# Optimization experiments

Measured on AMD Instinct MI355X. Metric: run time of the kernel, lower is better.

The kernel has to match this reference:

```python
import jax, jax.numpy as jnp
import numpy as np

N_SRC, N_DST, DEG = 100000, 50000, 16
NODE_IN, EDGE_IN, HID = 128, 64, 64
E = N_DST * DEG


def sparsemax(z):
    # z: [..., K]; sparsemax along last axis (Martins & Astudillo)
    z = z - jnp.max(z, axis=-1, keepdims=True)
    zs = -jnp.sort(-z, axis=-1)  # descending sort
    k_range = jnp.arange(1, z.shape[-1] + 1, dtype=z.dtype)
    cs = jnp.cumsum(zs, axis=-1)
    is_gt = (1.0 + k_range * zs > cs).astype(z.dtype)
    k = jnp.max(is_gt * k_range, axis=-1, keepdims=True)
    tau = (jnp.sum(is_gt * zs, axis=-1, keepdims=True) - 1.0) / k
    return jnp.maximum(z - tau, 0.0)


def setup_inputs() -> dict:
    key = jax.random.key(0)
    ks = jax.random.split(key, 8)
    s = 0.02
    return {
        "node_features": jax.random.normal(ks[0], (N_SRC, NODE_IN), jnp.float32),
        "edge_features": jax.random.normal(ks[1], (E, EDGE_IN), jnp.float32),
        "src_idx": jax.random.randint(ks[2], (E,), 0, N_SRC, jnp.int32),
        "We": s * jax.random.normal(ks[3], (EDGE_IN, HID), jnp.float32),
        "be": jnp.zeros((HID,), jnp.float32),
        "Wa": s * jax.random.normal(ks[4], (EDGE_IN, HID), jnp.float32),
        "ba": jnp.zeros((HID,), jnp.float32),
        "wa": s * jax.random.normal(ks[5], (HID,), jnp.float32),
        "Wo": s * jax.random.normal(ks[6], (NODE_IN + HID, HID), jnp.float32),
        "bo": jnp.zeros((HID,), jnp.float32),
        "Wn": s * jax.random.normal(ks[7], (NODE_IN + HID, HID), jnp.float32),
        "bn": jnp.zeros((HID,), jnp.float32),
        "n_dst": N_DST,
        "deg": DEG,
    }


def reference(node_features, edge_features, src_idx, We, be, Wa, ba, wa, Wo, bo, Wn, bn, n_dst, deg):
    # dropout is identity in eval / p=0
    h_dst = node_features[:n_dst]                               # [n_dst, node_in]
    # message_func: per-edge transforms
    e_out = jax.nn.relu(edge_features @ We + be)                # [E, hid]
    a = jax.nn.leaky_relu((edge_features @ Wa + ba) @ wa)       # [E]
    h_src_e = node_features[src_idx]                            # gather [E, node_in]
    m = jax.nn.relu(jnp.concatenate([h_src_e, e_out], axis=-1) @ Wo + bo)  # [E, hid]
    # reduce_func: mailbox is [n_dst, deg, .] (fixed in-degree graph)
    a = a.reshape(n_dst, deg)
    m = m.reshape(n_dst, deg, -1)
    alpha = sparsemax(a)                                        # [n_dst, deg]
    h_neigh = jnp.einsum('nd,ndh->nh', alpha, m)                # [n_dst, hid]
    # node update
    return jax.nn.relu(jnp.concatenate([h_dst, h_neigh], axis=-1) @ Wn + bn)
```

## Files before the change

kernel.cpp:

```cpp
#include <hip/hip_runtime.h>


#define ND 50000

typedef __bf16 bf16x8 __attribute__((ext_vector_type(8)));
typedef float f32x4 __attribute__((ext_vector_type(4)));

__device__ __forceinline__ void sync_wave() {
  asm volatile("s_waitcnt lgkmcnt(0)" ::: "memory");
}

__device__ __forceinline__ unsigned short f2bf(float x) {
  unsigned u = __float_as_uint(x);
  u += 0x7fffu + ((u >> 16) & 1u);
  return (unsigned short)(u >> 16);
}

union FragU { bf16x8 v; unsigned short u[8]; };

__device__ __forceinline__ bf16x8 ld_cvt8(const float* __restrict__ p, float* fr) {
  float4 f0 = *reinterpret_cast<const float4*>(p);
  float4 f1 = *reinterpret_cast<const float4*>(p + 4);
  fr[0]=f0.x; fr[1]=f0.y; fr[2]=f0.z; fr[3]=f0.w;
  fr[4]=f1.x; fr[5]=f1.y; fr[6]=f1.z; fr[7]=f1.w;
  FragU fu;
  #pragma unroll
  for (int j = 0; j < 8; ++j) fu.u[j] = f2bf(fr[j]);
  return fu.v;
}

extern "C" __global__ void gteast_prep(const float* __restrict__ Wa,
                                       const float* __restrict__ ba,
                                       const float* __restrict__ wa,
                                       float* __restrict__ vc) {
  const int k = threadIdx.x;
  if (k < 64) {
    float s = 0.f;
    for (int h = 0; h < 64; ++h) s += Wa[k * 64 + h] * wa[h];
    vc[k] = s;
  }
  if (k == 0) {
    float c = 0.f;
    for (int h = 0; h < 64; ++h) c += ba[h] * wa[h];
    vc[64] = c;
  }
}

#define MFMA(a, b, c) __builtin_amdgcn_mfma_f32_16x16x32_bf16((a), (b), (c), 0, 0, 0)

extern "C" __global__ void __launch_bounds__(256, 2)
gteast_edge(const float* __restrict__ nf, const float* __restrict__ ef,
            const int* __restrict__ src_idx,
            const float* __restrict__ We, const float* __restrict__ be,
            const float* __restrict__ Wo, const float* __restrict__ bo,
            const float* __restrict__ vc,
            float* __restrict__ hn_out) {
  __shared__ unsigned short WeT[64 * 72];
  __shared__ unsigned short WoT[64 * 200];
  __shared__ unsigned short Elds[4][16 * 72];

  const int tid = threadIdx.x;
  for (int i = tid; i < 64 * 64; i += 256) {
    int k = i >> 6, n = i & 63;
    WeT[n * 72 + k] = f2bf(We[i]);
  }
  for (int i = tid; i < 192 * 64; i += 256) {
    int k = i >> 6, n = i & 63;
    WoT[n * 200 + k] = f2bf(Wo[i]);
  }
  __syncthreads();

  const int lane = tid & 63, w = tid >> 6;
  const int q = lane >> 4, t = lane & 15;

  bf16x8 WeF[2][4], WoF[6][4];
  #pragma unroll
  for (int nt = 0; nt < 4; ++nt) {
    #pragma unroll
    for (int kc = 0; kc < 2; ++kc)
      WeF[kc][nt] = *reinterpret_cast<const bf16x8*>(&WeT[(nt * 16 + t) * 72 + kc * 32 + q * 8]);
    #pragma unroll
    for (int kc = 0; kc < 6; ++kc)
      WoF[kc][nt] = *reinterpret_cast<const bf16x8*>(&WoT[(nt * 16 + t) * 200 + kc * 32 + q * 8]);
  }
  float vsl[16];
  #pragma unroll
  for (int kc = 0; kc < 2; ++kc)
    for (int j = 0; j < 8; ++j) vsl[kc * 8 + j] = vc[kc * 32 + q * 8 + j];
  const float cval = vc[64];
  float beL[4], boL[4];
  #pragma unroll
  for (int nt = 0; nt < 4; ++nt) { beL[nt] = be[nt * 16 + t]; boL[nt] = bo[nt * 16 + t]; }

  unsigned short* E = Elds[w];
  const int wid = blockIdx.x * 4 + w;

  for (int it = 0; it < 8; ++it) {
    const int n = wid + it * 6252;
    if (n >= ND) continue;
    const long e0 = (long)n * 16;

    bf16x8 efr[2];
    float fr[8];
    float ap = 0.f;
    #pragma unroll
    for (int kc = 0; kc < 2; ++kc) {
      efr[kc] = ld_cvt8(ef + (e0 + t) * 64 + kc * 32 + q * 8, fr);
      #pragma unroll
      for (int j = 0; j < 8; ++j) ap += fr[j] * vsl[kc * 8 + j];
    }
    ap += __shfl_xor(ap, 16);
    ap += __shfl_xor(ap, 32);
    float a = ap + cval;
    a = a > 0.f ? a : 0.01f * a;

    #pragma unroll
    for (int nt = 0; nt < 4; ++nt) {
      f32x4 c = {0.f, 0.f, 0.f, 0.f};
      c = MFMA(efr[0], WeF[0][nt], c);
      c = MFMA(efr[1], WeF[1][nt], c);
      #pragma unroll
      for (int r = 0; r < 4; ++r) {
        float vv = fmaxf(c[r] + beL[nt], 0.f);
        E[(4 * q + r) * 72 + nt * 16 + t] = f2bf(vv);
      }
    }
    sync_wave();

    const int s = src_idx[e0 + t];
    const float* hp = nf + (long)s * 128;
    bf16x8 af[6];
    #pragma unroll
    for (int kc = 0; kc < 4; ++kc) af[kc] = ld_cvt8(hp + kc * 32 + q * 8, fr);
    af[4] = *reinterpret_cast<const bf16x8*>(&E[t * 72 + q * 8]);
    af[5] = *reinterpret_cast<const bf16x8*>(&E[t * 72 + 32 + q * 8]);

    f32x4 accM[4];
    #pragma unroll
    for (int nt = 0; nt < 4; ++nt) {
      f32x4 c = {0.f, 0.f, 0.f, 0.f};
      #pragma unroll
      for (int kc = 0; kc < 6; ++kc) c = MFMA(af[kc], WoF[kc][nt], c);
      #pragma unroll
      for (int r = 0; r < 4; ++r) c[r] = fmaxf(c[r] + boL[nt], 0.f);
      accM[nt] = c;
    }
    sync_wave();

    float z = a;
    #pragma unroll
    for (int k = 2; k <= 16; k <<= 1) {
      #pragma unroll
      for (int j = k >> 1; j > 0; j >>= 1) {
        float o = __shfl_xor(z, j);
        const bool upper = (t & j) != 0;
        const bool desc = (t & k) == 0;
        z = (upper != desc) ? fmaxf(z, o) : fminf(z, o);
      }
    }
    float cs = z;
    #pragma unroll
    for (int off = 1; off < 16; off <<= 1) {
      float o = __shfl_up(cs, off, 16);
      cs += (t >= off) ? o : 0.f;
    }
    const bool gt = 1.f + (float)(t + 1) * z > cs;
    float kf = gt ? (float)(t + 1) : 0.f;
    float sv = gt ? z : 0.f;
    #pragma unroll
    for (int m = 1; m < 16; m <<= 1) {
      kf = fmaxf(kf, __shfl_xor(kf, m));
      sv += __shfl_xor(sv, m);
    }
    const float tau = (sv - 1.f) / kf;
    const float alpha = fmaxf(a - tau, 0.f);

    float al[4];
    #pragma unroll
    for (int r = 0; r < 4; ++r) al[r] = __shfl(alpha, 4 * q + r);
    float p[4];
    #pragma unroll
    for (int nt = 0; nt < 4; ++nt) {
      p[nt] = al[0] * accM[nt][0] + al[1] * accM[nt][1] +
              al[2] * accM[nt][2] + al[3] * accM[nt][3];
      p[nt] += __shfl_xor(p[nt], 16);
      p[nt] += __shfl_xor(p[nt], 32);
    }
    const float pown = (q == 0) ? p[0] : (q == 1) ? p[1] : (q == 2) ? p[2] : p[3];
    hn_out[(long)n * 64 + lane] = pown;
  }
}

extern "C" __global__ void __launch_bounds__(256, 2)
gteast_out(const float* __restrict__ nf, const float* __restrict__ Wn,
           const float* __restrict__ bn, float* __restrict__ out) {
  __shared__ unsigned short WnT[64 * 200];
  const int tid = threadIdx.x;
  for (int i = tid; i < 192 * 64; i += 256) {
    int k = i >> 6, nn = i & 63;
    WnT[nn * 200 + k] = f2bf(Wn[i]);
  }
  __syncthreads();

  const int lane = tid & 63, w = tid >> 6, q = lane >> 4, t = lane & 15;
  bf16x8 WF[6][4];
  #pragma unroll
  for (int nt = 0; nt < 4; ++nt)
    #pragma unroll
    for (int kc = 0; kc < 6; ++kc)
      WF[kc][nt] = *reinterpret_cast<const bf16x8*>(&WnT[(nt * 16 + t) * 200 + kc * 32 + q * 8]);
  float bnL[4];
  #pragma unroll
  for (int nt = 0; nt < 4; ++nt) bnL[nt] = bn[nt * 16 + t];

  const int wid = blockIdx.x * 4 + w;
  for (int it = 0; it < 2; ++it) {
    const int tile = wid + it * 1564;
    const int r0 = tile * 16;
    if (r0 >= ND) continue;

    float fr[8];
    bf16x8 af[6];
    const float* hp = nf + (long)(r0 + t) * 128;
    #pragma unroll
    for (int kc = 0; kc < 4; ++kc) af[kc] = ld_cvt8(hp + kc * 32 + q * 8, fr);
    const float* gp = out + (long)(r0 + t) * 64;
    #pragma unroll
    for (int kc = 0; kc < 2; ++kc) af[4 + kc] = ld_cvt8(gp + kc * 32 + q * 8, fr);

    #pragma unroll
    for (int nt = 0; nt < 4; ++nt) {
      f32x4 c = {0.f, 0.f, 0.f, 0.f};
      #pragma unroll
      for (int kc = 0; kc < 6; ++kc) c = MFMA(af[kc], WF[kc][nt], c);
      #pragma unroll
      for (int r = 0; r < 4; ++r)
        out[(long)(r0 + 4 * q + r) * 64 + nt * 16 + t] = fmaxf(c[r] + bnL[nt], 0.f);
    }
  }
}

extern "C" void kernel_launch(void* const* d_in, const int* in_sizes, int n_in,
                              void* d_out, int out_size, void* d_ws, size_t ws_size,
                              hipStream_t stream) {
  const float* nf = (const float*)d_in[0];
  const float* ef = (const float*)d_in[1];
  const int* si   = (const int*)d_in[2];
  const float* We = (const float*)d_in[3];
  const float* be = (const float*)d_in[4];
  const float* Wa = (const float*)d_in[5];
  const float* ba = (const float*)d_in[6];
  const float* wa = (const float*)d_in[7];
  const float* Wo = (const float*)d_in[8];
  const float* bo = (const float*)d_in[9];
  const float* Wn = (const float*)d_in[10];
  const float* bn = (const float*)d_in[11];
  float* out = (float*)d_out;
  float* vc = (float*)d_ws;

  gteast_prep<<<1, 64, 0, stream>>>(Wa, ba, wa, vc);
  gteast_edge<<<1563, 256, 0, stream>>>(nf, ef, si, We, be, Wo, bo, vc, out);
  gteast_out<<<391, 256, 0, stream>>>(nf, Wn, bn, out);
}
```

Measured before the change: 418.5 us.

## Software-pipeline edge/neighbor loads, read weights from LDS, raise occupancy

The edge kernel now gives each wave 8 contiguous destination nodes instead of strided ones. It preloads the src indices once and prefetches the next iteration's edge features and gathered neighbor rows into registers while the current iteration computes. Weight fragments are read from LDS per MFMA instead of being held in registers, which frees VGPRs so launch bounds can go from 2 to 3 blocks per SIMD. Both kernels use a cheaper perm-based bf16 pack that rounds to nearest with ties away from zero instead of to even. The output kernel uses one tile per wave with twice as many blocks, and the prep kernel splits its dot products across 256 threads.

Result: faster. 387.5 us (-7.4%).

```diff
diff --git a/kernel.cpp b/kernel.cpp
--- a/kernel.cpp
+++ b/kernel.cpp
@@ -16,39 +16,41 @@
   return (unsigned short)(u >> 16);
 }
 
-union FragU { bf16x8 v; unsigned short u[8]; };
-
-__device__ __forceinline__ bf16x8 ld_cvt8(const float* __restrict__ p, float* fr) {
-  float4 f0 = *reinterpret_cast<const float4*>(p);
-  float4 f1 = *reinterpret_cast<const float4*>(p + 4);
-  fr[0]=f0.x; fr[1]=f0.y; fr[2]=f0.z; fr[3]=f0.w;
-  fr[4]=f1.x; fr[5]=f1.y; fr[6]=f1.z; fr[7]=f1.w;
-  FragU fu;
-  #pragma unroll
-  for (int j = 0; j < 8; ++j) fu.u[j] = f2bf(fr[j]);
-  return fu.v;
-}
+union Frag8 { bf16x8 v; unsigned u32[4]; };
+
+__device__ __forceinline__ bf16x8 pack8(const float* fr) {
+  Frag8 f;
+  #pragma unroll
+  for (int j = 0; j < 4; ++j) {
+    unsigned lo = __float_as_uint(fr[2 * j]) + 0x8000u;
+    unsigned hi = __float_as_uint(fr[2 * j + 1]) + 0x8000u;
+    f.u32[j] = __builtin_amdgcn_perm(hi, lo, 0x07060302);
+  }
+  return f.v;
+}
+
+#define MFMA(a, b, c) __builtin_amdgcn_mfma_f32_16x16x32_bf16((a), (b), (c), 0, 0, 0)
 
 extern "C" __global__ void gteast_prep(const float* __restrict__ Wa,
                                        const float* __restrict__ ba,
                                        const float* __restrict__ wa,
                                        float* __restrict__ vc) {
-  const int k = threadIdx.x;
-  if (k < 64) {
-    float s = 0.f;
-    for (int h = 0; h < 64; ++h) s += Wa[k * 64 + h] * wa[h];
-    vc[k] = s;
-  }
-  if (k == 0) {
-    float c = 0.f;
-    for (int h = 0; h < 64; ++h) c += ba[h] * wa[h];
-    vc[64] = c;
-  }
-}
-
-#define MFMA(a, b, c) __builtin_amdgcn_mfma_f32_16x16x32_bf16((a), (b), (c), 0, 0, 0)
-
-extern "C" __global__ void __launch_bounds__(256, 2)
+  __shared__ float red[260];
+  const int tid = threadIdx.x, k = tid >> 2, p = tid & 3;
+  float s = 0.f;
+  for (int h = 16 * p; h < 16 * p + 16; ++h) s += Wa[k * 64 + h] * wa[h];
+  red[tid] = s;
+  if (tid < 4) {
+    float sc = 0.f;
+    for (int h = 16 * tid; h < 16 * tid + 16; ++h) sc += ba[h] * wa[h];
+    red[256 + tid] = sc;
+  }
+  __syncthreads();
+  if (p == 0) vc[k] = red[4 * k] + red[4 * k + 1] + red[4 * k + 2] + red[4 * k + 3];
+  if (tid == 0) vc[64] = red[256] + red[257] + red[258] + red[259];
+}
+
+extern "C" __global__ void __launch_bounds__(256, 3)
 gteast_edge(const float* __restrict__ nf, const float* __restrict__ ef,
             const int* __restrict__ src_idx,
             const float* __restrict__ We, const float* __restrict__ be,
@@ -58,6 +60,7 @@
   __shared__ unsigned short WeT[64 * 72];
   __shared__ unsigned short WoT[64 * 200];
   __shared__ unsigned short Elds[4][16 * 72];
+  __shared__ float vls[68];
 
   const int tid = threadIdx.x;
   for (int i = tid; i < 64 * 64; i += 256) {
@@ -68,57 +71,80 @@
     int k = i >> 6, n = i & 63;
     WoT[n * 200 + k] = f2bf(Wo[i]);
   }
+  if (tid < 65) vls[tid] = vc[tid];
   __syncthreads();
 
   const int lane = tid & 63, w = tid >> 6;
   const int q = lane >> 4, t = lane & 15;
-
-  bf16x8 WeF[2][4], WoF[6][4];
-  #pragma unroll
-  for (int nt = 0; nt < 4; ++nt) {
-    #pragma unroll
-    for (int kc = 0; kc < 2; ++kc)
-      WeF[kc][nt] = *reinterpret_cast<const bf16x8*>(&WeT[(nt * 16 + t) * 72 + kc * 32 + q * 8]);
-    #pragma unroll
-    for (int kc = 0; kc < 6; ++kc)
-      WoF[kc][nt] = *reinterpret_cast<const bf16x8*>(&WoT[(nt * 16 + t) * 200 + kc * 32 + q * 8]);
-  }
+  const int wid = blockIdx.x * 4 + w;
+  if (wid * 8 >= ND) return;
+
+  unsigned short* E = Elds[w];
+  const float cval = vls[64];
+  float beL[4], boL[4];
+  #pragma unroll
+  for (int nt = 0; nt < 4; ++nt) { beL[nt] = be[nt * 16 + t]; boL[nt] = bo[nt * 16 + t]; }
   float vsl[16];
   #pragma unroll
-  for (int kc = 0; kc < 2; ++kc)
-    for (int j = 0; j < 8; ++j) vsl[kc * 8 + j] = vc[kc * 32 + q * 8 + j];
-  const float cval = vc[64];
-  float beL[4], boL[4];
-  #pragma unroll
-  for (int nt = 0; nt < 4; ++nt) { beL[nt] = be[nt * 16 + t]; boL[nt] = bo[nt * 16 + t]; }
-
-  unsigned short* E = Elds[w];
-  const int wid = blockIdx.x * 4 + w;
+  for (int j = 0; j < 8; ++j) { vsl[j] = vls[q * 8 + j]; vsl[8 + j] = vls[32 + q * 8 + j]; }
+
+  const int si0 = src_idx[wid * 128 + lane];
+  const int si1 = src_idx[wid * 128 + 64 + lane];
+
+  const long ebase = (long)(wid * 128);
+
+  float4 efn[4];
+  {
+    const float* er = ef + (ebase + t) * 64 + q * 8;
+    efn[0] = *reinterpret_cast<const float4*>(er);
+    efn[1] = *reinterpret_cast<const float4*>(er + 4);
+    efn[2] = *reinterpret_cast<const float4*>(er + 32);
+    efn[3] = *reinterpret_cast<const float4*>(er + 36);
+  }
+  float hraw[32];
+  {
+    const int s0 = __shfl(si0, t);
+    const float* hp = nf + (long)s0 * 128 + q * 8;
+    #pragma unroll
+    for (int kc = 0; kc < 4; ++kc) {
+      float4 a0 = *reinterpret_cast<const float4*>(hp + kc * 32);
+      float4 a1 = *reinterpret_cast<const float4*>(hp + kc * 32 + 4);
+      hraw[kc * 8 + 0] = a0.x; hraw[kc * 8 + 1] = a0.y; hraw[kc * 8 + 2] = a0.z; hraw[kc * 8 + 3] = a0.w;
+      hraw[kc * 8 + 4] = a1.x; hraw[kc * 8 + 5] = a1.y; hraw[kc * 8 + 6] = a1.z; hraw[kc * 8 + 7] = a1.w;
+    }
+  }
 
   for (int it = 0; it < 8; ++it) {
-    const int n = wid + it * 6252;
-    if (n >= ND) continue;
-    const long e0 = (long)n * 16;
-
-    bf16x8 efr[2];
-    float fr[8];
+    const int n = wid * 8 + it;
+    const int itn = it < 7 ? it + 1 : 7;
+
+    float fe[16];
+    fe[0] = efn[0].x; fe[1] = efn[0].y; fe[2] = efn[0].z; fe[3] = efn[0].w;
+    fe[4] = efn[1].x; fe[5] = efn[1].y; fe[6] = efn[1].z; fe[7] = efn[1].w;
+    fe[8] = efn[2].x; fe[9] = efn[2].y; fe[10] = efn[2].z; fe[11] = efn[2].w;
+    fe[12] = efn[3].x; fe[13] = efn[3].y; fe[14] = efn[3].z; fe[15] = efn[3].w;
+    {
+      const float* er = ef + (ebase + itn * 16 + t) * 64 + q * 8;
+      efn[0] = *reinterpret_cast<const float4*>(er);
+      efn[1] = *reinterpret_cast<const float4*>(er + 4);
+      efn[2] = *reinterpret_cast<const float4*>(er + 32);
+      efn[3] = *reinterpret_cast<const float4*>(er + 36);
+    }
+
     float ap = 0.f;
     #pragma unroll
-    for (int kc = 0; kc < 2; ++kc) {
-      efr[kc] = ld_cvt8(ef + (e0 + t) * 64 + kc * 32 + q * 8, fr);
-      #pragma unroll
-      for (int j = 0; j < 8; ++j) ap += fr[j] * vsl[kc * 8 + j];
-    }
+    for (int j = 0; j < 16; ++j) ap += fe[j] * vsl[j];
     ap += __shfl_xor(ap, 16);
     ap += __shfl_xor(ap, 32);
     float a = ap + cval;
     a = a > 0.f ? a : 0.01f * a;
 
+    const bf16x8 e0 = pack8(fe), e1 = pack8(fe + 8);
     #pragma unroll
     for (int nt = 0; nt < 4; ++nt) {
       f32x4 c = {0.f, 0.f, 0.f, 0.f};
-      c = MFMA(efr[0], WeF[0][nt], c);
-      c = MFMA(efr[1], WeF[1][nt], c);
+      c = MFMA(e0, *reinterpret_cast<const bf16x8*>(&WeT[(nt * 16 + t) * 72 + q * 8]), c);
+      c = MFMA(e1, *reinterpret_cast<const bf16x8*>(&WeT[(nt * 16 + t) * 72 + 32 + q * 8]), c);
       #pragma unroll
       for (int r = 0; r < 4; ++r) {
         float vv = fmaxf(c[r] + beL[nt], 0.f);
@@ -127,20 +153,32 @@
     }
     sync_wave();
 
-    const int s = src_idx[e0 + t];
-    const float* hp = nf + (long)s * 128;
     bf16x8 af[6];
     #pragma unroll
-    for (int kc = 0; kc < 4; ++kc) af[kc] = ld_cvt8(hp + kc * 32 + q * 8, fr);
+    for (int kc = 0; kc < 4; ++kc) af[kc] = pack8(hraw + kc * 8);
     af[4] = *reinterpret_cast<const bf16x8*>(&E[t * 72 + q * 8]);
     af[5] = *reinterpret_cast<const bf16x8*>(&E[t * 72 + 32 + q * 8]);
 
+    {
+      const int sn = (itn < 4) ? __shfl(si0, 16 * itn + t)
+                               : __shfl(si1, 16 * (itn - 4) + t);
+      const float* hp = nf + (long)sn * 128 + q * 8;
+      #pragma unroll
+      for (int kc = 0; kc < 4; ++kc) {
+        float4 a0 = *reinterpret_cast<const float4*>(hp + kc * 32);
+        float4 a1 = *reinterpret_cast<const float4*>(hp + kc * 32 + 4);
+        hraw[kc * 8 + 0] = a0.x; hraw[kc * 8 + 1] = a0.y; hraw[kc * 8 + 2] = a0.z; hraw[kc * 8 + 3] = a0.w;
+        hraw[kc * 8 + 4] = a1.x; hraw[kc * 8 + 5] = a1.y; hraw[kc * 8 + 6] = a1.z; hraw[kc * 8 + 7] = a1.w;
+      }
+    }
+
     f32x4 accM[4];
     #pragma unroll
     for (int nt = 0; nt < 4; ++nt) {
       f32x4 c = {0.f, 0.f, 0.f, 0.f};
       #pragma unroll
-      for (int kc = 0; kc < 6; ++kc) c = MFMA(af[kc], WoF[kc][nt], c);
+      for (int kc = 0; kc < 6; ++kc)
+        c = MFMA(af[kc], *reinterpret_cast<const bf16x8*>(&WoT[(nt * 16 + t) * 200 + kc * 32 + q * 8]), c);
       #pragma unroll
       for (int r = 0; r < 4; ++r) c[r] = fmaxf(c[r] + boL[nt], 0.f);
       accM[nt] = c;
@@ -191,7 +229,7 @@
   }
 }
 
-extern "C" __global__ void __launch_bounds__(256, 2)
+extern "C" __global__ void __launch_bounds__(256, 3)
 gteast_out(const float* __restrict__ nf, const float* __restrict__ Wn,
            const float* __restrict__ bn, float* __restrict__ out) {
   __shared__ unsigned short WnT[64 * 200];
@@ -203,40 +241,44 @@
   __syncthreads();
 
   const int lane = tid & 63, w = tid >> 6, q = lane >> 4, t = lane & 15;
-  bf16x8 WF[6][4];
-  #pragma unroll
-  for (int nt = 0; nt < 4; ++nt)
+  const int tile = blockIdx.x * 4 + w;
+  if (tile >= ND / 16) return;
+  const int r0 = tile * 16;
+
+  float bnL[4];
+  #pragma unroll
+  for (int nt = 0; nt < 4; ++nt) bnL[nt] = bn[nt * 16 + t];
+
+  float raw[8];
+  bf16x8 af[6];
+  const float* hp = nf + (long)(r0 + t) * 128 + q * 8;
+  #pragma unroll
+  for (int kc = 0; kc < 4; ++kc) {
+    float4 a0 = *reinterpret_cast<const float4*>(hp + kc * 32);
+    float4 a1 = *reinterpret_cast<const float4*>(hp + kc * 32 + 4);
+    raw[0] = a0.x; raw[1] = a0.y; raw[2] = a0.z; raw[3] = a0.w;
+    raw[4] = a1.x; raw[5] = a1.y; raw[6] = a1.z; raw[7] = a1.w;
+    af[kc] = pack8(raw);
+  }
+  const float* gp = out + (long)(r0 + t) * 64 + q * 8;
+  #pragma unroll
+  for (int kc = 0; kc < 2; ++kc) {
+    float4 a0 = *reinterpret_cast<const float4*>(gp + kc * 32);
+    float4 a1 = *reinterpret_cast<const float4*>(gp + kc * 32 + 4);
+    raw[0] = a0.x; raw[1] = a0.y; raw[2] = a0.z; raw[3] = a0.w;
+    raw[4] = a1.x; raw[5] = a1.y; raw[6] = a1.z; raw[7] = a1.w;
+    af[4 + kc] = pack8(raw);
+  }
+
+  #pragma unroll
+  for (int nt = 0; nt < 4; ++nt) {
+    f32x4 c = {0.f, 0.f, 0.f, 0.f};
     #pragma unroll
     for (int kc = 0; kc < 6; ++kc)
-      WF[kc][nt] = *reinterpret_cast<const bf16x8*>(&WnT[(nt * 16 + t) * 200 + kc * 32 + q * 8]);
-  float bnL[4];
-  #pragma unroll
-  for (int nt = 0; nt < 4; ++nt) bnL[nt] = bn[nt * 16 + t];
-
-  const int wid = blockIdx.x * 4 + w;
-  for (int it = 0; it < 2; ++it) {
-    const int tile = wid + it * 1564;
-    const int r0 = tile * 16;
-    if (r0 >= ND) continue;
-
-    float fr[8];
-    bf16x8 af[6];
-    const float* hp = nf + (long)(r0 + t) * 128;
-    #pragma unroll
-    for (int kc = 0; kc < 4; ++kc) af[kc] = ld_cvt8(hp + kc * 32 + q * 8, fr);
-    const float* gp = out + (long)(r0 + t) * 64;
-    #pragma unroll
-    for (int kc = 0; kc < 2; ++kc) af[4 + kc] = ld_cvt8(gp + kc * 32 + q * 8, fr);
-
-    #pragma unroll
-    for (int nt = 0; nt < 4; ++nt) {
-      f32x4 c = {0.f, 0.f, 0.f, 0.f};
-      #pragma unroll
-      for (int kc = 0; kc < 6; ++kc) c = MFMA(af[kc], WF[kc][nt], c);
-      #pragma unroll
-      for (int r = 0; r < 4; ++r)
-        out[(long)(r0 + 4 * q + r) * 64 + nt * 16 + t] = fmaxf(c[r] + bnL[nt], 0.f);
-    }
+      c = MFMA(af[kc], *reinterpret_cast<const bf16x8*>(&WnT[(nt * 16 + t) * 200 + kc * 32 + q * 8]), c);
+    #pragma unroll
+    for (int r = 0; r < 4; ++r)
+      out[(long)(r0 + 4 * q + r) * 64 + nt * 16 + t] = fmaxf(c[r] + bnL[nt], 0.f);
   }
 }
 
@@ -258,7 +300,7 @@
   float* out = (float*)d_out;
   float* vc = (float*)d_ws;
 
-  gteast_prep<<<1, 64, 0, stream>>>(Wa, ba, wa, vc);
+  gteast_prep<<<1, 256, 0, stream>>>(Wa, ba, wa, vc);
   gteast_edge<<<1563, 256, 0, stream>>>(nf, ef, si, We, be, Wo, bo, vc, out);
-  gteast_out<<<391, 256, 0, stream>>>(nf, Wn, bn, out);
-}
+  gteast_out<<<782, 256, 0, stream>>>(nf, Wn, bn, out);
+}
```
